# Kernel tuning notes

Hardware: AMD Instinct MI355X
Metric: run time of the kernel (lower is better)

## Reference

```python
import jax, jax.numpy as jnp
import numpy as np

NUM_HEADS = 8
WINDOW = 8


def _sdpa(q, k, v, scale):
    # q,k,v: (..., heads, S, d)
    scores = jnp.einsum('...sd,...td->...st', q, k) * scale
    p = jax.nn.softmax(scores, axis=-1)
    return jnp.einsum('...st,...td->...sd', p, v)


def setup_inputs() -> dict:
    key = jax.random.key(0)
    k1, k2, k3 = jax.random.split(key, 3)
    B, Himg, Wimg, C = 8, 128, 128, 256
    x = jax.random.normal(k1, (B, Himg * Wimg, C), dtype=jnp.float32)
    W_qkv = jax.random.normal(k2, (C, 3 * C), dtype=jnp.float32) * (C ** -0.5)
    W_proj = jax.random.normal(k3, (C, C), dtype=jnp.float32) * (C ** -0.5)
    b_proj = jnp.zeros((C,), dtype=jnp.float32)
    return {"x": x, "W_qkv": W_qkv, "W_proj": W_proj, "b_proj": b_proj, "H": Himg, "W": Wimg}


def reference(x, W_qkv, W_proj, b_proj, H, W):
    B, N, C = x.shape
    nh, ws = NUM_HEADS, WINDOW
    hd = C // nh
    scale = hd ** -0.5
    split = nh // 2  # local heads = global heads = nh/2

    x4 = x.reshape(B, H, W, C)
    pad_r = (ws - W % ws) % ws
    pad_b = (ws - H % ws) % ws
    if pad_r > 0 or pad_b > 0:
        x4 = jnp.pad(x4, ((0, 0), (0, pad_b), (0, pad_r), (0, 0)))
    Hp, Wp = x4.shape[1], x4.shape[2]

    qkv = (x4 @ W_qkv).reshape(B, Hp, Wp, 3, nh, hd)
    q, k, v = qkv[..., 0, :, :], qkv[..., 1, :, :], qkv[..., 2, :, :]  # (B,Hp,Wp,nh,hd)

    nwh, nww = Hp // ws, Wp // ws

    def win_part(t):
        # (B,Hp,Wp,h,d) -> (B,nwh,nww,h,ws*ws,d)
        h = t.shape[3]
        t = t.reshape(B, nwh, ws, nww, ws, h, hd)
        return t.transpose(0, 1, 3, 5, 2, 4, 6).reshape(B, nwh, nww, h, ws * ws, hd)

    def win_rev(t):
        # (B,nwh,nww,h,ws*ws,d) -> (B,Hp,Wp,h*d)
        h = t.shape[3]
        t = t.reshape(B, nwh, nww, h, ws, ws, hd)
        return t.transpose(0, 1, 4, 2, 5, 3, 6).reshape(B, Hp, Wp, h * hd)

    def grid_part(t):
        # (B,Hp,Wp,h,d) -> (B,ws,ws,h,nwh*nww,d)
        h = t.shape[3]
        t = t.reshape(B, nwh, ws, nww, ws, h, hd)
        return t.transpose(0, 2, 4, 5, 1, 3, 6).reshape(B, ws, ws, h, nwh * nww, hd)

    def grid_rev(t):
        # (B,ws,ws,h,nwh*nww,d) -> (B,Hp,Wp,h*d)
        h = t.shape[3]
        t = t.reshape(B, ws, ws, h, nwh, nww, hd)
        return t.transpose(0, 4, 1, 5, 2, 3, 6).reshape(B, Hp, Wp, h * hd)

    # local branch: first half of heads, window attention
    out_local = win_rev(_sdpa(win_part(q[..., :split, :]),
                              win_part(k[..., :split, :]),
                              win_part(v[..., :split, :]), scale))
    # global branch: second half of heads, grid attention
    out_global = grid_rev(_sdpa(grid_part(q[..., split:, :]),
                                grid_part(k[..., split:, :]),
                                grid_part(v[..., split:, :]), scale))

    out = jnp.concatenate([out_local, out_global], axis=-1)
    if pad_r > 0 or pad_b > 0:
        out = out[:, :H, :W, :]
    out = out.reshape(B, N, C)
    return out @ W_proj + b_proj
```

## Files before the change

kernel.cpp:

```cpp
#include <hip/hip_runtime.h>
#include <hip/hip_bf16.h>

using bf16x8 = __attribute__((ext_vector_type(8))) short;
using f32x4  = __attribute__((ext_vector_type(4))) float;

#define MFMA16(a, b, c) __builtin_amdgcn_mfma_f32_16x16x32_bf16((a), (b), (c), 0, 0, 0)

__device__ __forceinline__ short f2b(float f) {
    unsigned u = __builtin_bit_cast(unsigned, f);
    u = (u + 0x7fffu + ((u >> 16) & 1u)) >> 16;
    return (short)u;
}
__device__ __forceinline__ short pkb(float f) {
    return (short)((__builtin_bit_cast(unsigned, f) + 0x8000u) >> 16);
}
__device__ __forceinline__ void gl_lds16(const short* g, short* l) {
    __builtin_amdgcn_global_load_lds(
        (const __attribute__((address_space(1))) unsigned int*)g,
        (__attribute__((address_space(3))) unsigned int*)l, 16, 0, 0);
}

__global__ __launch_bounds__(256)
void cast_x_kernel(const float* __restrict__ x, short* __restrict__ xb) {
    const int i = blockIdx.x * 256 + threadIdx.x;
    const float4 v = ((const float4*)x)[i];
    short4 o;
    o.x = f2b(v.x); o.y = f2b(v.y); o.z = f2b(v.z); o.w = f2b(v.w);
    ((short4*)xb)[i] = o;
}

__global__ __launch_bounds__(256)
void cast_w_kernel(const float* __restrict__ wqkv, const float* __restrict__ wproj,
                   short* __restrict__ wqT, short* __restrict__ wpT) {
    const int t = blockIdx.x * 256 + threadIdx.x;
    if (t < 768 * 256) {
        const int n = t >> 8, k = t & 255;
        float v = wqkv[k * 768 + n];
        if (n < 256) v *= 0.17677669529663687f;
        wqT[t] = f2b(v);
    } else {
        const int u = t - 768 * 256;
        const int n = u >> 8, k = u & 255;
        wpT[u] = f2b(wproj[k * 256 + n]);
    }
}

template <int LDN, bool BF16OUT>
__global__ __launch_bounds__(256)
void gemm_kernel(const short* __restrict__ A, const short* __restrict__ Bt,
                 void* __restrict__ Cout, const float* __restrict__ bias) {
    __shared__ short As[128 * 32];
    __shared__ short Bs[128 * 32];
    const int tid  = threadIdx.x;
    const int lane = tid & 63, wave = tid >> 6;
    const int wm = wave >> 1, wn = wave & 1;
    const int quad = lane >> 4, l16 = lane & 15;
    const int m0 = blockIdx.y * 128;
    const int n0 = blockIdx.x * 128;

    const f32x4 zf = {0.f, 0.f, 0.f, 0.f};
    f32x4 acc[4][4];
#pragma unroll
    for (int i = 0; i < 4; ++i)
#pragma unroll
        for (int j = 0; j < 4; ++j) acc[i][j] = zf;

    const int srow = wave * 16 + (lane >> 2);
    const int scol = (lane & 3) * 8;
    const short* Ap = A  + (long)(m0 + srow) * 256 + scol;
    const short* Bp = Bt + (long)(n0 + srow) * 256 + scol;
    short* lA = &As[wave * 512];
    short* lB = &Bs[wave * 512];

    for (int kt = 0; kt < 8; ++kt) {
        const int off = kt * 32;
        __syncthreads();
        gl_lds16(Ap + off,            lA);
        gl_lds16(Ap + 64 * 256 + off, lA + 2048);
        gl_lds16(Bp + off,            lB);
        gl_lds16(Bp + 64 * 256 + off, lB + 2048);
        __syncthreads();
        bf16x8 af[4], bfr[4];
#pragma unroll
        for (int i = 0; i < 4; ++i)
            af[i] = *(const bf16x8*)&As[(wm * 64 + i * 16 + l16) * 32 + quad * 8];
#pragma unroll
        for (int j = 0; j < 4; ++j)
            bfr[j] = *(const bf16x8*)&Bs[(wn * 64 + j * 16 + l16) * 32 + quad * 8];
#pragma unroll
        for (int i = 0; i < 4; ++i)
#pragma unroll
            for (int j = 0; j < 4; ++j)
                acc[i][j] = MFMA16(af[i], bfr[j], acc[i][j]);
    }

    if constexpr (BF16OUT) {
        short* C = (short*)Cout;
#pragma unroll
        for (int i = 0; i < 4; ++i)
#pragma unroll
            for (int r = 0; r < 4; ++r) {
                const long row = m0 + wm * 64 + i * 16 + quad * 4 + r;
#pragma unroll
                for (int j = 0; j < 4; ++j)
                    C[row * LDN + n0 + wn * 64 + j * 16 + l16] = pkb(acc[i][j][r]);
            }
    } else {
        float* C = (float*)Cout;
#pragma unroll
        for (int i = 0; i < 4; ++i)
#pragma unroll
            for (int r = 0; r < 4; ++r) {
                const long row = m0 + wm * 64 + i * 16 + quad * 4 + r;
#pragma unroll
                for (int j = 0; j < 4; ++j) {
                    const int col = n0 + wn * 64 + j * 16 + l16;
                    C[row * LDN + col] = acc[i][j][r] + bias[col];
                }
            }
    }
}

__global__ __launch_bounds__(256)
void local_attn_kernel(const short* __restrict__ qkv, short* __restrict__ attn) {
    __shared__ short sVT[4][32 * 72];
    __shared__ short sP[4][16 * 72];
    const int tid  = threadIdx.x;
    const int lane = tid & 63, wave = tid >> 6;
    const int quad = lane >> 4, l16 = lane & 15;
    const int sh   = blockIdx.x * 4 + wave;
    const int head = sh & 3;
    const int win  = (sh >> 2) & 255;
    const int b    = sh >> 10;
    const int base_tok = b * 16384 + (win >> 4) * 1024 + (win & 15) * 8;
    const int ch = head * 32;

    {
        const int tok = base_tok + (lane >> 3) * 128 + (lane & 7);
        const short* vrow = qkv + (long)tok * 768 + 512 + ch;
        bf16x8 v0 = *(const bf16x8*)(vrow + 0);
        bf16x8 v1 = *(const bf16x8*)(vrow + 8);
        bf16x8 v2 = *(const bf16x8*)(vrow + 16);
        bf16x8 v3 = *(const bf16x8*)(vrow + 24);
#pragma unroll
        for (int d = 0; d < 8; ++d) {
            sVT[wave][(d     ) * 72 + lane] = v0[d];
            sVT[wave][(d +  8) * 72 + lane] = v1[d];
            sVT[wave][(d + 16) * 72 + lane] = v2[d];
            sVT[wave][(d + 24) * 72 + lane] = v3[d];
        }
    }

    bf16x8 aq[4], bk[4];
#pragma unroll
    for (int i = 0; i < 4; ++i) {
        const int s = i * 16 + l16;
        const int tok = base_tok + (s >> 3) * 128 + (s & 7);
        aq[i] = *(const bf16x8*)(qkv + (long)tok * 768 + ch + quad * 8);
    }
#pragma unroll
    for (int j = 0; j < 4; ++j) {
        const int t = j * 16 + l16;
        const int tok = base_tok + (t >> 3) * 128 + (t & 7);
        bk[j] = *(const bf16x8*)(qkv + (long)tok * 768 + 256 + ch + quad * 8);
    }

    bf16x8 vb[2][2];
#pragma unroll
    for (int kk = 0; kk < 2; ++kk)
#pragma unroll
        for (int j2 = 0; j2 < 2; ++j2)
            vb[kk][j2] = *(const bf16x8*)&sVT[wave][(j2 * 16 + l16) * 72 + kk * 32 + quad * 8];

    const bf16x8 vone = {0x3F80, 0x3F80, 0x3F80, 0x3F80, 0x3F80, 0x3F80, 0x3F80, 0x3F80};
    const f32x4 zf = {0.f, 0.f, 0.f, 0.f};

#pragma unroll
    for (int i = 0; i < 4; ++i) {
        f32x4 sa[4] = {zf, zf, zf, zf};
#pragma unroll
        for (int j = 0; j < 4; ++j)
            sa[j] = MFMA16(aq[i], bk[j], sa[j]);
#pragma unroll
        for (int j = 0; j < 4; ++j)
#pragma unroll
            for (int r = 0; r < 4; ++r)
                sP[wave][(quad * 4 + r) * 72 + j * 16 + l16] = pkb(__expf(sa[j][r]));

        f32x4 o0 = zf, o1 = zf, os = zf;
#pragma unroll
        for (int kk = 0; kk < 2; ++kk) {
            const bf16x8 pa = *(const bf16x8*)&sP[wave][l16 * 72 + kk * 32 + quad * 8];
            o0 = MFMA16(pa, vb[kk][0], o0);
            o1 = MFMA16(pa, vb[kk][1], o1);
            os = MFMA16(pa, vone, os);
        }
#pragma unroll
        for (int r = 0; r < 4; ++r) {
            const int s = i * 16 + quad * 4 + r;
            const int tok = base_tok + (s >> 3) * 128 + (s & 7);
            const float inv = 1.f / os[r];
            attn[(long)tok * 256 + ch + l16]      = pkb(o0[r] * inv);
            attn[(long)tok * 256 + ch + 16 + l16] = pkb(o1[r] * inv);
        }
    }
}

__global__ __launch_bounds__(256)
void global_attn_kernel(const short* __restrict__ qkv, short* __restrict__ attn) {
    __shared__ short sVT[32 * 264];
    __shared__ short sP[4][16 * 72];
    const int tid  = threadIdx.x;
    const int lane = tid & 63, wave = tid >> 6;
    const int quad = lane >> 4, l16 = lane & 15;
    const int sh   = blockIdx.x;
    const int head = sh & 3;
    const int pos  = (sh >> 2) & 63;
    const int b    = sh >> 8;
    const int base_tok = b * 16384 + (pos >> 3) * 128 + (pos & 7);
    const int ch = (4 + head) * 32;

    {
        const int s = tid;
        const int tok = base_tok + (s >> 4) * 1024 + (s & 15) * 8;
        const short* vrow = qkv + (long)tok * 768 + 512 + ch;
        bf16x8 v0 = *(const bf16x8*)(vrow + 0);
        bf16x8 v1 = *(const bf16x8*)(vrow + 8);
        bf16x8 v2 = *(const bf16x8*)(vrow + 16);
        bf16x8 v3 = *(const bf16x8*)(vrow + 24);
#pragma unroll
        for (int d = 0; d < 8; ++d) {
            sVT[(d     ) * 264 + s] = v0[d];
            sVT[(d +  8) * 264 + s] = v1[d];
            sVT[(d + 16) * 264 + s] = v2[d];
            sVT[(d + 24) * 264 + s] = v3[d];
        }
    }
    __syncthreads();

    bf16x8 aq[4];
#pragma unroll
    for (int i = 0; i < 4; ++i) {
        const int s = wave * 64 + i * 16 + l16;
        const int tok = base_tok + (s >> 4) * 1024 + (s & 15) * 8;
        aq[i] = *(const bf16x8*)(qkv + (long)tok * 768 + ch + quad * 8);
    }

    const bf16x8 vone = {0x3F80, 0x3F80, 0x3F80, 0x3F80, 0x3F80, 0x3F80, 0x3F80, 0x3F80};
    const f32x4 zf = {0.f, 0.f, 0.f, 0.f};
    f32x4 o0[4], o1[4], os[4];
#pragma unroll
    for (int i = 0; i < 4; ++i) { o0[i] = zf; o1[i] = zf; os[i] = zf; }

    for (int nc = 0; nc < 4; ++nc) {
        bf16x8 bk[4];
#pragma unroll
        for (int j = 0; j < 4; ++j) {
            const int t = nc * 64 + j * 16 + l16;
            const int tok = base_tok + (t >> 4) * 1024 + (t & 15) * 8;
            bk[j] = *(const bf16x8*)(qkv + (long)tok * 768 + 256 + ch + quad * 8);
        }
        bf16x8 vb[2][2];
#pragma unroll
        for (int kk = 0; kk < 2; ++kk)
#pragma unroll
            for (int j2 = 0; j2 < 2; ++j2)
                vb[kk][j2] = *(const bf16x8*)&sVT[(j2 * 16 + l16) * 264 + nc * 64 + kk * 32 + quad * 8];

#pragma unroll
        for (int i = 0; i < 4; ++i) {
            f32x4 sa[4] = {zf, zf, zf, zf};
#pragma unroll
            for (int j = 0; j < 4; ++j)
                sa[j] = MFMA16(aq[i], bk[j], sa[j]);
#pragma unroll
            for (int j = 0; j < 4; ++j)
#pragma unroll
                for (int r = 0; r < 4; ++r)
                    sP[wave][(quad * 4 + r) * 72 + j * 16 + l16] = pkb(__expf(sa[j][r]));
#pragma unroll
            for (int kk = 0; kk < 2; ++kk) {
                const bf16x8 pa = *(const bf16x8*)&sP[wave][l16 * 72 + kk * 32 + quad * 8];
                o0[i] = MFMA16(pa, vb[kk][0], o0[i]);
                o1[i] = MFMA16(pa, vb[kk][1], o1[i]);
                os[i] = MFMA16(pa, vone, os[i]);
            }
        }
    }

#pragma unroll
    for (int i = 0; i < 4; ++i)
#pragma unroll
        for (int r = 0; r < 4; ++r) {
            const int s = wave * 64 + i * 16 + quad * 4 + r;
            const int tok = base_tok + (s >> 4) * 1024 + (s & 15) * 8;
            const float inv = 1.f / os[i][r];
            attn[(long)tok * 256 + ch + l16]      = pkb(o0[i][r] * inv);
            attn[(long)tok * 256 + ch + 16 + l16] = pkb(o1[i][r] * inv);
        }
}

extern "C" void kernel_launch(void* const* d_in, const int* in_sizes, int n_in,
                              void* d_out, int out_size, void* d_ws, size_t ws_size,
                              hipStream_t stream) {
    const float* x     = (const float*)d_in[0];
    const float* wqkv  = (const float*)d_in[1];
    const float* wproj = (const float*)d_in[2];
    const float* bproj = (const float*)d_in[3];

    char* ws = (char*)d_ws;
    short* xb   = (short*)(ws);
    short* wqT  = (short*)(ws +  67108864);
    short* wpT  = (short*)(ws +  67502080);
    short* qkv  = (short*)(ws +  67633152);
    short* attn = (short*)(ws + 268959744);
    float* out  = (float*)d_out;

    cast_x_kernel<<<dim3(32768), dim3(256), 0, stream>>>(x, xb);
    cast_w_kernel<<<dim3(1024), dim3(256), 0, stream>>>(wqkv, wproj, wqT, wpT);
    gemm_kernel<768, true><<<dim3(6, 1024), dim3(256), 0, stream>>>(xb, wqT, (void*)qkv, nullptr);
    local_attn_kernel<<<dim3(2048), dim3(256), 0, stream>>>(qkv, attn);
    global_attn_kernel<<<dim3(2048), dim3(256), 0, stream>>>(qkv, attn);
    gemm_kernel<256, false><<<dim3(2, 1024), dim3(256), 0, stream>>>(attn, wpT, (void*)out, bproj);
}
```

Baseline: 467.4 us.

## Write QKV in window/grid-partitioned layout and remap GEMM block order

The QKV GEMM epilogue now scatters outputs directly into per-(batch, window/grid, head) contiguous buffers for local and global branches, so the attention kernels read Q/K/V with contiguous loads instead of strided token gathers. The GEMMs use a 1D grid with XCD-aware block swizzling, and output stores are packed to 32-bit pairs via lane shuffles. Extra __syncthreads calls were added around the per-wave sP scratch usage, which costs some synchronisation overhead. The scattered epilogue writes may be less coalesced than the row-major stores they replace.

After: 483.5 us. 3.4% more time.

```diff
diff --git a/kernel.cpp b/kernel.cpp
--- a/kernel.cpp
+++ b/kernel.cpp
@@ -13,6 +13,9 @@
 }
 __device__ __forceinline__ short pkb(float f) {
     return (short)((__builtin_bit_cast(unsigned, f) + 0x8000u) >> 16);
+}
+__device__ __forceinline__ unsigned pk2(float lo, float hi) {
+    return (unsigned)(unsigned short)pkb(lo) | ((unsigned)(unsigned short)pkb(hi) << 16);
 }
 __device__ __forceinline__ void gl_lds16(const short* g, short* l) {
     __builtin_amdgcn_global_load_lds(
@@ -45,18 +48,19 @@
     }
 }
 
-template <int LDN, bool BF16OUT>
-__global__ __launch_bounds__(256)
-void gemm_kernel(const short* __restrict__ A, const short* __restrict__ Bt,
-                 void* __restrict__ Cout, const float* __restrict__ bias) {
+__global__ __launch_bounds__(256)
+void gemm_qkv_kernel(const short* __restrict__ A, const short* __restrict__ Bt,
+                     short* __restrict__ qkvL, short* __restrict__ qkvG) {
     __shared__ short As[128 * 32];
     __shared__ short Bs[128 * 32];
     const int tid  = threadIdx.x;
     const int lane = tid & 63, wave = tid >> 6;
     const int wm = wave >> 1, wn = wave & 1;
     const int quad = lane >> 4, l16 = lane & 15;
-    const int m0 = blockIdx.y * 128;
-    const int n0 = blockIdx.x * 128;
+    const int id = blockIdx.x;
+    const int qq = id >> 3, xcd = id & 7;
+    const int m0 = (xcd * 128 + qq / 6) * 128;
+    const int n0 = (qq % 6) * 128;
 
     const f32x4 zf = {0.f, 0.f, 0.f, 0.f};
     f32x4 acc[4][4];
@@ -94,35 +98,123 @@
                 acc[i][j] = MFMA16(af[i], bfr[j], acc[i][j]);
     }
 
-    if constexpr (BF16OUT) {
-        short* C = (short*)Cout;
+    const int part = n0 >> 8;
+    const bool isLocal = ((n0 >> 7) & 1) == 0;
+    const bool evenL = (l16 & 1) == 0;
+    if (isLocal) {
+        short* base = qkvL + part * 2048;
 #pragma unroll
         for (int i = 0; i < 4; ++i)
 #pragma unroll
             for (int r = 0; r < 4; ++r) {
-                const long row = m0 + wm * 64 + i * 16 + quad * 4 + r;
-#pragma unroll
-                for (int j = 0; j < 4; ++j)
-                    C[row * LDN + n0 + wn * 64 + j * 16 + l16] = pkb(acc[i][j][r]);
+                const int token = m0 + wm * 64 + i * 16 + quad * 4 + r;
+                const int b = token >> 14, hw = token & 16383;
+                const int hrow = hw >> 7, wcol = hw & 127;
+                const int win = ((hrow >> 3) << 4) + (wcol >> 3);
+                const int ti  = ((hrow & 7) << 3) + (wcol & 7);
+                const long shb = (long)((b << 8) + win) << 2;
+#pragma unroll
+                for (int j = 0; j < 4; ++j) {
+                    const float v = acc[i][j][r];
+                    const float w = __shfl_xor(v, 1);
+                    if (evenL) {
+                        const int c128 = wn * 64 + j * 16 + l16;
+                        const int head = c128 >> 5, ch = c128 & 31;
+                        *(unsigned*)&base[(shb + head) * 6144 + ti * 32 + ch] = pk2(v, w);
+                    }
+                }
             }
     } else {
-        float* C = (float*)Cout;
+        short* base = qkvG + part * 8192;
 #pragma unroll
         for (int i = 0; i < 4; ++i)
 #pragma unroll
             for (int r = 0; r < 4; ++r) {
-                const long row = m0 + wm * 64 + i * 16 + quad * 4 + r;
+                const int token = m0 + wm * 64 + i * 16 + quad * 4 + r;
+                const int b = token >> 14, hw = token & 16383;
+                const int hrow = hw >> 7, wcol = hw & 127;
+                const int pos = ((hrow & 7) << 3) + (wcol & 7);
+                const int ti  = ((hrow >> 3) << 4) + (wcol >> 3);
+                const long shb = (long)((b << 6) + pos) << 2;
 #pragma unroll
                 for (int j = 0; j < 4; ++j) {
-                    const int col = n0 + wn * 64 + j * 16 + l16;
-                    C[row * LDN + col] = acc[i][j][r] + bias[col];
+                    const float v = acc[i][j][r];
+                    const float w = __shfl_xor(v, 1);
+                    if (evenL) {
+                        const int c128 = wn * 64 + j * 16 + l16;
+                        const int head = c128 >> 5, ch = c128 & 31;
+                        *(unsigned*)&base[(shb + head) * 24576 + ti * 32 + ch] = pk2(v, w);
+                    }
                 }
             }
     }
 }
 
 __global__ __launch_bounds__(256)
-void local_attn_kernel(const short* __restrict__ qkv, short* __restrict__ attn) {
+void gemm_proj_kernel(const short* __restrict__ A, const short* __restrict__ Bt,
+                      float* __restrict__ C, const float* __restrict__ bias) {
+    __shared__ short As[128 * 32];
+    __shared__ short Bs[128 * 32];
+    const int tid  = threadIdx.x;
+    const int lane = tid & 63, wave = tid >> 6;
+    const int wm = wave >> 1, wn = wave & 1;
+    const int quad = lane >> 4, l16 = lane & 15;
+    const int id = blockIdx.x;
+    const int qq = id >> 3, xcd = id & 7;
+    const int m0 = (xcd * 128 + (qq >> 1)) * 128;
+    const int n0 = (qq & 1) * 128;
+
+    const f32x4 zf = {0.f, 0.f, 0.f, 0.f};
+    f32x4 acc[4][4];
+#pragma unroll
+    for (int i = 0; i < 4; ++i)
+#pragma unroll
+        for (int j = 0; j < 4; ++j) acc[i][j] = zf;
+
+    const int srow = wave * 16 + (lane >> 2);
+    const int scol = (lane & 3) * 8;
+    const short* Ap = A  + (long)(m0 + srow) * 256 + scol;
+    const short* Bp = Bt + (long)(n0 + srow) * 256 + scol;
+    short* lA = &As[wave * 512];
+    short* lB = &Bs[wave * 512];
+
+    for (int kt = 0; kt < 8; ++kt) {
+        const int off = kt * 32;
+        __syncthreads();
+        gl_lds16(Ap + off,            lA);
+        gl_lds16(Ap + 64 * 256 + off, lA + 2048);
+        gl_lds16(Bp + off,            lB);
+        gl_lds16(Bp + 64 * 256 + off, lB + 2048);
+        __syncthreads();
+        bf16x8 af[4], bfr[4];
+#pragma unroll
+        for (int i = 0; i < 4; ++i)
+            af[i] = *(const bf16x8*)&As[(wm * 64 + i * 16 + l16) * 32 + quad * 8];
+#pragma unroll
+        for (int j = 0; j < 4; ++j)
+            bfr[j] = *(const bf16x8*)&Bs[(wn * 64 + j * 16 + l16) * 32 + quad * 8];
+#pragma unroll
+        for (int i = 0; i < 4; ++i)
+#pragma unroll
+            for (int j = 0; j < 4; ++j)
+                acc[i][j] = MFMA16(af[i], bfr[j], acc[i][j]);
+    }
+
+#pragma unroll
+    for (int i = 0; i < 4; ++i)
+#pragma unroll
+        for (int r = 0; r < 4; ++r) {
+            const long row = m0 + wm * 64 + i * 16 + quad * 4 + r;
+#pragma unroll
+            for (int j = 0; j < 4; ++j) {
+                const int col = n0 + wn * 64 + j * 16 + l16;
+                C[row * 256 + col] = acc[i][j][r] + bias[col];
+            }
+        }
+}
+
+__global__ __launch_bounds__(256)
+void local_attn_kernel(const short* __restrict__ qkvL, short* __restrict__ attn) {
     __shared__ short sVT[4][32 * 72];
     __shared__ short sP[4][16 * 72];
     const int tid  = threadIdx.x;
@@ -134,14 +226,15 @@
     const int b    = sh >> 10;
     const int base_tok = b * 16384 + (win >> 4) * 1024 + (win & 15) * 8;
     const int ch = head * 32;
+    const short* qb = qkvL + (long)sh * 6144;
+    const short* kb = qb + 2048;
+    const short* vp = qb + 4096;
 
     {
-        const int tok = base_tok + (lane >> 3) * 128 + (lane & 7);
-        const short* vrow = qkv + (long)tok * 768 + 512 + ch;
-        bf16x8 v0 = *(const bf16x8*)(vrow + 0);
-        bf16x8 v1 = *(const bf16x8*)(vrow + 8);
-        bf16x8 v2 = *(const bf16x8*)(vrow + 16);
-        bf16x8 v3 = *(const bf16x8*)(vrow + 24);
+        bf16x8 v0 = *(const bf16x8*)(vp + lane * 32);
+        bf16x8 v1 = *(const bf16x8*)(vp + lane * 32 + 8);
+        bf16x8 v2 = *(const bf16x8*)(vp + lane * 32 + 16);
+        bf16x8 v3 = *(const bf16x8*)(vp + lane * 32 + 24);
 #pragma unroll
         for (int d = 0; d < 8; ++d) {
             sVT[wave][(d     ) * 72 + lane] = v0[d];
@@ -150,30 +243,26 @@
             sVT[wave][(d + 24) * 72 + lane] = v3[d];
         }
     }
+    __syncthreads();
 
     bf16x8 aq[4], bk[4];
 #pragma unroll
-    for (int i = 0; i < 4; ++i) {
-        const int s = i * 16 + l16;
-        const int tok = base_tok + (s >> 3) * 128 + (s & 7);
-        aq[i] = *(const bf16x8*)(qkv + (long)tok * 768 + ch + quad * 8);
-    }
-#pragma unroll
-    for (int j = 0; j < 4; ++j) {
-        const int t = j * 16 + l16;
-        const int tok = base_tok + (t >> 3) * 128 + (t & 7);
-        bk[j] = *(const bf16x8*)(qkv + (long)tok * 768 + 256 + ch + quad * 8);
-    }
-
-    bf16x8 vb[2][2];
+    for (int i = 0; i < 4; ++i)
+        aq[i] = *(const bf16x8*)(qb + (i * 16 + l16) * 32 + quad * 8);
+#pragma unroll
+    for (int j = 0; j < 4; ++j)
+        bk[j] = *(const bf16x8*)(kb + (j * 16 + l16) * 32 + quad * 8);
+
+    bf16x8 vbf[2][2];
 #pragma unroll
     for (int kk = 0; kk < 2; ++kk)
 #pragma unroll
         for (int j2 = 0; j2 < 2; ++j2)
-            vb[kk][j2] = *(const bf16x8*)&sVT[wave][(j2 * 16 + l16) * 72 + kk * 32 + quad * 8];
+            vbf[kk][j2] = *(const bf16x8*)&sVT[wave][(j2 * 16 + l16) * 72 + kk * 32 + quad * 8];
 
     const bf16x8 vone = {0x3F80, 0x3F80, 0x3F80, 0x3F80, 0x3F80, 0x3F80, 0x3F80, 0x3F80};
     const f32x4 zf = {0.f, 0.f, 0.f, 0.f};
+    const bool evenL = (l16 & 1) == 0;
 
 #pragma unroll
     for (int i = 0; i < 4; ++i) {
@@ -186,28 +275,35 @@
 #pragma unroll
             for (int r = 0; r < 4; ++r)
                 sP[wave][(quad * 4 + r) * 72 + j * 16 + l16] = pkb(__expf(sa[j][r]));
+        __syncthreads();
 
         f32x4 o0 = zf, o1 = zf, os = zf;
 #pragma unroll
         for (int kk = 0; kk < 2; ++kk) {
             const bf16x8 pa = *(const bf16x8*)&sP[wave][l16 * 72 + kk * 32 + quad * 8];
-            o0 = MFMA16(pa, vb[kk][0], o0);
-            o1 = MFMA16(pa, vb[kk][1], o1);
+            o0 = MFMA16(pa, vbf[kk][0], o0);
+            o1 = MFMA16(pa, vbf[kk][1], o1);
             os = MFMA16(pa, vone, os);
         }
+        __syncthreads();
+
 #pragma unroll
         for (int r = 0; r < 4; ++r) {
             const int s = i * 16 + quad * 4 + r;
             const int tok = base_tok + (s >> 3) * 128 + (s & 7);
             const float inv = 1.f / os[r];
-            attn[(long)tok * 256 + ch + l16]      = pkb(o0[r] * inv);
-            attn[(long)tok * 256 + ch + 16 + l16] = pkb(o1[r] * inv);
-        }
-    }
-}
-
-__global__ __launch_bounds__(256)
-void global_attn_kernel(const short* __restrict__ qkv, short* __restrict__ attn) {
+            const float a0 = o0[r] * inv, a1 = o1[r] * inv;
+            const float b0 = __shfl_xor(a0, 1), b1 = __shfl_xor(a1, 1);
+            if (evenL) {
+                *(unsigned*)&attn[(long)tok * 256 + ch + l16]      = pk2(a0, b0);
+                *(unsigned*)&attn[(long)tok * 256 + ch + 16 + l16] = pk2(a1, b1);
+            }
+        }
+    }
+}
+
+__global__ __launch_bounds__(256)
+void global_attn_kernel(const short* __restrict__ qkvG, short* __restrict__ attn) {
     __shared__ short sVT[32 * 264];
     __shared__ short sP[4][16 * 72];
     const int tid  = threadIdx.x;
@@ -219,32 +315,29 @@
     const int b    = sh >> 8;
     const int base_tok = b * 16384 + (pos >> 3) * 128 + (pos & 7);
     const int ch = (4 + head) * 32;
+    const short* qb = qkvG + (long)sh * 24576;
+    const short* kb = qb + 8192;
+    const short* vp = qb + 16384;
 
     {
-        const int s = tid;
-        const int tok = base_tok + (s >> 4) * 1024 + (s & 15) * 8;
-        const short* vrow = qkv + (long)tok * 768 + 512 + ch;
-        bf16x8 v0 = *(const bf16x8*)(vrow + 0);
-        bf16x8 v1 = *(const bf16x8*)(vrow + 8);
-        bf16x8 v2 = *(const bf16x8*)(vrow + 16);
-        bf16x8 v3 = *(const bf16x8*)(vrow + 24);
+        bf16x8 v0 = *(const bf16x8*)(vp + tid * 32);
+        bf16x8 v1 = *(const bf16x8*)(vp + tid * 32 + 8);
+        bf16x8 v2 = *(const bf16x8*)(vp + tid * 32 + 16);
+        bf16x8 v3 = *(const bf16x8*)(vp + tid * 32 + 24);
 #pragma unroll
         for (int d = 0; d < 8; ++d) {
-            sVT[(d     ) * 264 + s] = v0[d];
-            sVT[(d +  8) * 264 + s] = v1[d];
-            sVT[(d + 16) * 264 + s] = v2[d];
-            sVT[(d + 24) * 264 + s] = v3[d];
+            sVT[(d     ) * 264 + tid] = v0[d];
+            sVT[(d +  8) * 264 + tid] = v1[d];
+            sVT[(d + 16) * 264 + tid] = v2[d];
+            sVT[(d + 24) * 264 + tid] = v3[d];
         }
     }
     __syncthreads();
 
     bf16x8 aq[4];
 #pragma unroll
-    for (int i = 0; i < 4; ++i) {
-        const int s = wave * 64 + i * 16 + l16;
-        const int tok = base_tok + (s >> 4) * 1024 + (s & 15) * 8;
-        aq[i] = *(const bf16x8*)(qkv + (long)tok * 768 + ch + quad * 8);
-    }
+    for (int i = 0; i < 4; ++i)
+        aq[i] = *(const bf16x8*)(qb + (wave * 64 + i * 16 + l16) * 32 + quad * 8);
 
     const bf16x8 vone = {0x3F80, 0x3F80, 0x3F80, 0x3F80, 0x3F80, 0x3F80, 0x3F80, 0x3F80};
     const f32x4 zf = {0.f, 0.f, 0.f, 0.f};
@@ -255,17 +348,14 @@
     for (int nc = 0; nc < 4; ++nc) {
         bf16x8 bk[4];
 #pragma unroll
-        for (int j = 0; j < 4; ++j) {
-            const int t = nc * 64 + j * 16 + l16;
-            const int tok = base_tok + (t >> 4) * 1024 + (t & 15) * 8;
-            bk[j] = *(const bf16x8*)(qkv + (long)tok * 768 + 256 + ch + quad * 8);
-        }
-        bf16x8 vb[2][2];
+        for (int j = 0; j < 4; ++j)
+            bk[j] = *(const bf16x8*)(kb + (nc * 64 + j * 16 + l16) * 32 + quad * 8);
+        bf16x8 vbf[2][2];
 #pragma unroll
         for (int kk = 0; kk < 2; ++kk)
 #pragma unroll
             for (int j2 = 0; j2 < 2; ++j2)
-                vb[kk][j2] = *(const bf16x8*)&sVT[(j2 * 16 + l16) * 264 + nc * 64 + kk * 32 + quad * 8];
+                vbf[kk][j2] = *(const bf16x8*)&sVT[(j2 * 16 + l16) * 264 + nc * 64 + kk * 32 + quad * 8];
 
 #pragma unroll
         for (int i = 0; i < 4; ++i) {
@@ -278,16 +368,19 @@
 #pragma unroll
                 for (int r = 0; r < 4; ++r)
                     sP[wave][(quad * 4 + r) * 72 + j * 16 + l16] = pkb(__expf(sa[j][r]));
+            __syncthreads();
 #pragma unroll
             for (int kk = 0; kk < 2; ++kk) {
                 const bf16x8 pa = *(const bf16x8*)&sP[wave][l16 * 72 + kk * 32 + quad * 8];
-                o0[i] = MFMA16(pa, vb[kk][0], o0[i]);
-                o1[i] = MFMA16(pa, vb[kk][1], o1[i]);
+                o0[i] = MFMA16(pa, vbf[kk][0], o0[i]);
+                o1[i] = MFMA16(pa, vbf[kk][1], o1[i]);
                 os[i] = MFMA16(pa, vone, os[i]);
             }
-        }
-    }
-
+            __syncthreads();
+        }
+    }
+
+    const bool evenL = (l16 & 1) == 0;
 #pragma unroll
     for (int i = 0; i < 4; ++i)
 #pragma unroll
@@ -295,8 +388,12 @@
             const int s = wave * 64 + i * 16 + quad * 4 + r;
             const int tok = base_tok + (s >> 4) * 1024 + (s & 15) * 8;
             const float inv = 1.f / os[i][r];
-            attn[(long)tok * 256 + ch + l16]      = pkb(o0[i][r] * inv);
-            attn[(long)tok * 256 + ch + 16 + l16] = pkb(o1[i][r] * inv);
+            const float a0 = o0[i][r] * inv, a1 = o1[i][r] * inv;
+            const float b0 = __shfl_xor(a0, 1), b1 = __shfl_xor(a1, 1);
+            if (evenL) {
+                *(unsigned*)&attn[(long)tok * 256 + ch + l16]      = pk2(a0, b0);
+                *(unsigned*)&attn[(long)tok * 256 + ch + 16 + l16] = pk2(a1, b1);
+            }
         }
 }
 
@@ -312,14 +409,15 @@
     short* xb   = (short*)(ws);
     short* wqT  = (short*)(ws +  67108864);
     short* wpT  = (short*)(ws +  67502080);
-    short* qkv  = (short*)(ws +  67633152);
+    short* qkvL = (short*)(ws +  67633152);
+    short* qkvG = (short*)(ws + 168296448);
     short* attn = (short*)(ws + 268959744);
     float* out  = (float*)d_out;
 
     cast_x_kernel<<<dim3(32768), dim3(256), 0, stream>>>(x, xb);
     cast_w_kernel<<<dim3(1024), dim3(256), 0, stream>>>(wqkv, wproj, wqT, wpT);
-    gemm_kernel<768, true><<<dim3(6, 1024), dim3(256), 0, stream>>>(xb, wqT, (void*)qkv, nullptr);
-    local_attn_kernel<<<dim3(2048), dim3(256), 0, stream>>>(qkv, attn);
-    global_attn_kernel<<<dim3(2048), dim3(256), 0, stream>>>(qkv, attn);
-    gemm_kernel<256, false><<<dim3(2, 1024), dim3(256), 0, stream>>>(attn, wpT, (void*)out, bproj);
-}
+    gemm_qkv_kernel<<<dim3(6144), dim3(256), 0, stream>>>(xb, wqT, qkvL, qkvG);
+    local_attn_kernel<<<dim3(2048), dim3(256), 0, stream>>>(qkvL, attn);
+    global_attn_kernel<<<dim3(2048), dim3(256), 0, stream>>>(qkvG, attn);
+    gemm_proj_kernel<<<dim3(2048), dim3(256), 0, stream>>>(attn, wpT, out, bproj);
+}
```
